# Kernel tuning notes

Measured on AMD Instinct MI355X. Metric: run time of the kernel, lower is better.

Reference implementation:

```python
import jax, jax.numpy as jnp
import numpy as np

B, BOUNDS, NRIM, K, UNITS = 4096, 512, 6, 4, 600
H_IN, DK_IN, DV_IN = 4, 64, 400
H_C, DK_C, DV_C = 4, 32, 100


def setup_inputs() -> dict:
    key = jax.random.key(0)
    ks = jax.random.split(key, 16)
    s = 0.02
    return {
        'inputs': jax.random.normal(ks[0], (B, BOUNDS + NRIM), jnp.float32),
        'hs': jax.random.normal(ks[1], (B, NRIM, UNITS), jnp.float32) * s,
        'cs': jax.random.normal(ks[2], (B, NRIM, UNITS), jnp.float32) * s,
        'Wk': jax.random.normal(ks[3], (BOUNDS, H_IN * DK_IN), jnp.float32) * s,
        'bk': jnp.zeros((H_IN * DK_IN,), jnp.float32),
        'Wv': jax.random.normal(ks[4], (BOUNDS, H_IN * DV_IN), jnp.float32) * s,
        'bv': jnp.zeros((H_IN * DV_IN,), jnp.float32),
        'Wq': jax.random.normal(ks[5], (NRIM, UNITS, H_IN * DK_IN), jnp.float32) * s,
        'lstm_k': jax.random.normal(ks[6], (NRIM, DV_IN, 4 * UNITS), jnp.float32) * s,
        'lstm_r': jax.random.normal(ks[7], (NRIM, UNITS, 4 * UNITS), jnp.float32) * s,
        'lstm_b': jnp.zeros((NRIM, 4 * UNITS), jnp.float32),
        'Wkc': jax.random.normal(ks[8], (NRIM, UNITS, H_C * DK_C), jnp.float32) * s,
        'Wvc': jax.random.normal(ks[9], (NRIM, UNITS, H_C * DV_C), jnp.float32) * s,
        'Wqc': jax.random.normal(ks[10], (NRIM, UNITS, H_C * DK_C), jnp.float32) * s,
        'Wout': jax.random.normal(ks[11], (NRIM, H_C * DV_C, UNITS), jnp.float32) * s,
    }


def _split_heads(t, n_heads, d_head):
    # [B, T, n_heads*d_head] -> [B, n_heads, T, d_head] (matches tf.split+stack)
    b, t_len = t.shape[0], t.shape[1]
    return t.reshape(b, t_len, n_heads, d_head).transpose(0, 2, 1, 3)


def reference(inputs, hs, cs, Wk, bk, Wv, bv, Wq, lstm_k, lstm_r, lstm_b, Wkc, Wvc, Wqc, Wout):
    x = inputs[:, :BOUNDS]                                   # [B, bounds]
    rim_dist = inputs[:, BOUNDS:BOUNDS + NRIM]               # [B, nRIM]

    # ---- input attention ----
    xx = jnp.stack([x, jnp.zeros_like(x)], axis=1)           # [B, 2, bounds]
    k_lay = xx @ Wk + bk                                     # [B, 2, H*dk]
    v_lay = xx @ Wv + bv                                     # [B, 2, H*dv]
    q_lay = jnp.einsum('bnu,nuo->bno', hs, Wq)               # grouped linear [B, nRIM, H*dq]
    kh = _split_heads(k_lay, H_IN, DK_IN)                    # [B, H, 2, dk]
    vh = _split_heads(v_lay, H_IN, DV_IN)                    # [B, H, 2, dv]
    qh = _split_heads(q_lay, H_IN, DK_IN)                    # [B, H, nRIM, dk]
    v2 = vh.mean(axis=1)                                     # [B, 2, dv]
    scores = jnp.einsum('bhnd,bhtd->bhnt', qh, kh) / np.sqrt(DK_IN).astype(np.float32)
    scores2 = scores.mean(axis=1)                            # [B, nRIM, 2]

    # top-k RIM selection mask from RIM_dist (use_attn=False path)
    _, idx = jax.lax.top_k(rim_dist, K)                      # [B, K]
    mask = jnp.zeros((inputs.shape[0], NRIM), inputs.dtype)
    mask = mask.at[jnp.arange(inputs.shape[0])[:, None], idx].set(1.0)[..., None]  # [B, nRIM, 1]

    probs = jax.nn.softmax(scores2, axis=-1)                 # dropout inactive (training=False)
    rnn_in = jnp.einsum('bnt,btv->bnv', probs, v2) * mask    # [B, nRIM, dv]

    # ---- grouped LSTM (keras gate order i,f,c,o) ----
    gates = (jnp.einsum('bnv,nvo->bno', rnn_in, lstm_k)
             + jnp.einsum('bnu,nuo->bno', hs, lstm_r) + lstm_b)  # [B, nRIM, 4*units]
    i, f, g, o = jnp.split(gates, 4, axis=-1)
    c_rnn = jax.nn.sigmoid(f) * cs + jax.nn.sigmoid(i) * jnp.tanh(g)
    h_rnn = jax.nn.sigmoid(o) * jnp.tanh(c_rnn)
    h_new = jax.lax.stop_gradient(h_rnn * (1.0 - mask)) + h_rnn * mask

    # ---- communication attention among RIMs ----
    kc = _split_heads(jnp.einsum('bnu,nuo->bno', h_new, Wkc), H_C, DK_C)  # [B, Hc, nRIM, dkc]
    vc = _split_heads(jnp.einsum('bnu,nuo->bno', h_new, Wvc), H_C, DV_C)
    qc = _split_heads(jnp.einsum('bnu,nuo->bno', h_new, Wqc), H_C, DK_C)
    sc = jnp.einsum('bhnd,bhmd->bhnm', qc, kc) / np.sqrt(DK_C).astype(np.float32)
    pc = jax.nn.softmax(sc, axis=-1) * mask[:, None, :, :]   # zero rows of inactive query RIMs
    ctx = jnp.einsum('bhnm,bhmv->bhnv', pc, vc)              # [B, Hc, nRIM, dvc]
    ctx = ctx.transpose(0, 2, 1, 3).reshape(inputs.shape[0], NRIM, H_C * DV_C)
    h_comm = jnp.einsum('bno,nou->bnu', ctx, Wout) + h_new   # grouped output proj + residual

    # ---- masked state update ----
    h_upd = h_comm * mask + hs * (1.0 - mask)
    c_upd = c_rnn * mask + cs * (1.0 - mask)
    out_state = h_upd.reshape(inputs.shape[0], UNITS * NRIM)
    return out_state, h_upd, c_upd
```

## Files before the change

### kernel.cpp

```cpp
#include <hip/hip_runtime.h>

namespace {
typedef unsigned short u16;
typedef __attribute__((ext_vector_type(8))) __bf16 bf16x8;
typedef __attribute__((ext_vector_type(4))) float f32x4;

constexpr long long kB  = 4096;
constexpr long long kOS = kB * 3600;

constexpr size_t oWkvT  = 0;
constexpr size_t oWqT   = oWkvT  + 768ull*512*2;
constexpr size_t oWcomT = oWqT   + 6ull*256*608*2;
constexpr size_t oWoutT = oWcomT + 6ull*768*608*2;
constexpr size_t oLstmT = oWoutT + 6ull*640*416*2;
constexpr size_t oBp    = oLstmT + 6ull*2432*1024*2;
constexpr size_t oBkv   = oBp    + 6ull*2432*4;
constexpr size_t oZero  = oBkv   + 768*4;
constexpr size_t oMask  = oZero  + 256;
constexpr size_t oArena = oMask  + 4096ull*6*4;
constexpr size_t oHs2   = oArena;
constexpr size_t oRnn   = oHs2  + (4096ull*3600+64)*2;
constexpr size_t oKV    = oRnn  + 4096ull*2400*2;
constexpr size_t oXbf   = oKV   + 4096ull*768*2;
constexpr size_t oQlay  = oXbf;
constexpr size_t oCqv   = oArena;
constexpr size_t oCtx   = oCqv  + 4096ull*4608*2;
}

__device__ __forceinline__ u16 f2b(float f) {
  union { float f; unsigned u; } x; x.f = f;
  unsigned r = (x.u + 0x7fffu + ((x.u >> 16) & 1u)) >> 16;
  return (u16)r;
}
__device__ __forceinline__ float b2f(u16 u) {
  union { unsigned u; float f; } x; x.u = ((unsigned)u) << 16;
  return x.f;
}
__device__ __forceinline__ float sigmoidf_(float x) { return 1.f / (1.f + __expf(-x)); }
__device__ __forceinline__ float tanhf_(float x) {
  const float e = __expf(2.f * x);
  return 1.f - 2.f / (e + 1.f);
}

__device__ __forceinline__ void gload16(const void* g, void* l) {
  __builtin_amdgcn_global_load_lds((const __attribute__((address_space(1))) void*)g,
                                   (__attribute__((address_space(3))) void*)l, 16, 0, 0);
}
__device__ __forceinline__ void vmcnt0_barrier() {
  asm volatile("s_waitcnt vmcnt(0)" ::: "memory");
  __builtin_amdgcn_s_barrier();
}

union FragU { uint2 u2[2]; bf16x8 v; };

template<int MODE>
__global__ __launch_bounds__(256) void gemm128(
    const u16* __restrict__ A, int lda, int strideA,
    const u16* __restrict__ A2, int lda2, int strideA2,
    const u16* __restrict__ Bt, long strideB, int Kpad,
    void* __restrict__ C, int ldc, int strideC,
    const float* __restrict__ bias, int strideBias,
    int N, int nks, int storeBf16, int nx, int swz,
    const u16* __restrict__ zerobuf,
    const float* __restrict__ cs, const float* __restrict__ mask,
    float* __restrict__ c_upd, float* __restrict__ h_upd, u16* __restrict__ hnbf,
    const float* __restrict__ hs_in, float* __restrict__ out_state)
{
  __shared__ __align__(16) u16 As0[128 * 32];
  __shared__ __align__(16) u16 Bs0[128 * 32];
  __shared__ __align__(16) u16 As1[128 * 32];
  __shared__ __align__(16) u16 Bs1[128 * 32];

  const int nwg = gridDim.x;
  const int orig = blockIdx.x;
  const int q = nwg >> 3, r = nwg & 7;
  const int xcd = orig & 7, bidx = orig >> 3;
  const int wgid = (xcd < r ? xcd * (q + 1) : r * (q + 1) + (xcd - r) * q) + bidx;
  int xt, mt, rim;
  if (swz == 0) {
    xt = wgid % nx;
    const int t2 = wgid / nx;
    mt = t2 & 31;
    rim = t2 >> 5;
  } else {
    const int g = wgid / 320;
    const int rem = wgid % 320;
    rim = g >> 1;
    mt = rem / 10;
    xt = (g & 1) * 10 + rem % 10;
    if (xt >= 19) return;
  }
  const int m0 = mt * 128, n0 = xt * 128;

  A += (size_t)rim * strideA;
  if (MODE == 2) A2 += (size_t)rim * strideA2;
  Bt += (size_t)rim * strideB;
  if (bias) bias += (size_t)rim * strideBias;

  const int t = threadIdx.x;
  const int w = t >> 6, lane = t & 63;
  const int lrow = lane & 15, lk = lane >> 4;
  const int wr = w >> 1, wc = w & 1;

  f32x4 acc[4][4] = {};

  const int rA0 = t >> 2,         cA0 = (t & 3) ^ ((rA0 >> 1) & 3);
  const int rA1 = (t + 256) >> 2, cA1 = (t & 3) ^ ((rA1 >> 1) & 3);

  auto stage = [&](int s, u16* Asd, u16* Bsd) {
    const int k0 = s * 32;
    const int gk0 = k0 + cA0 * 8, gk1 = k0 + cA1 * 8;
    const u16 *p0, *p1;
    if (MODE == 2) {
      p0 = (gk0 < 400)  ? A  + (size_t)(m0 + rA0) * lda  + gk0
         : (gk0 < 1000) ? A2 + (size_t)(m0 + rA0) * lda2 + (gk0 - 400)
                        : zerobuf;
      p1 = (gk1 < 400)  ? A  + (size_t)(m0 + rA1) * lda  + gk1
         : (gk1 < 1000) ? A2 + (size_t)(m0 + rA1) * lda2 + (gk1 - 400)
                        : zerobuf;
    } else {
      p0 = A + (size_t)(m0 + rA0) * lda + gk0;
      p1 = A + (size_t)(m0 + rA1) * lda + gk1;
    }
    gload16(p0, Asd + (size_t)t * 8);
    gload16(p1, Asd + (size_t)(t + 256) * 8);
    gload16(Bt + (size_t)(n0 + rA0) * Kpad + k0 + cA0 * 8, Bsd + (size_t)t * 8);
    gload16(Bt + (size_t)(n0 + rA1) * Kpad + k0 + cA1 * 8, Bsd + (size_t)(t + 256) * 8);
  };

  auto compute = [&](const u16* Asrc, const u16* Bsrc, int snext, u16* Asd, u16* Bsd, bool donext) {
    FragU af[4], bfr[4];
#pragma unroll
    for (int mf = 0; mf < 4; ++mf) {
      const int rr = wr * 64 + mf * 16 + lrow;
      const int sw = ((rr >> 1) & 3) << 4;
      const char* base = (const char*)Asrc + rr * 64;
      af[mf].u2[0] = *(const uint2*)(base + ((8 * lk) ^ sw));
      af[mf].u2[1] = *(const uint2*)(base + ((8 * lk + 32) ^ sw));
    }
#pragma unroll
    for (int nf = 0; nf < 4; ++nf) {
      const int rr = wc * 64 + nf * 16 + lrow;
      const int sw = ((rr >> 1) & 3) << 4;
      const char* base = (const char*)Bsrc + rr * 64;
      bfr[nf].u2[0] = *(const uint2*)(base + ((8 * lk) ^ sw));
      bfr[nf].u2[1] = *(const uint2*)(base + ((8 * lk + 32) ^ sw));
    }
    if (donext) stage(snext, Asd, Bsd);
#pragma unroll
    for (int mf = 0; mf < 4; ++mf)
#pragma unroll
      for (int nf = 0; nf < 4; ++nf)
        acc[mf][nf] = __builtin_amdgcn_mfma_f32_16x16x32_bf16(af[mf].v, bfr[nf].v, acc[mf][nf], 0, 0, 0);
    vmcnt0_barrier();
  };

  stage(0, As0, Bs0);
  vmcnt0_barrier();
  int s = 0;
  for (; s + 2 <= nks; s += 2) {
    compute(As0, Bs0, s + 1, As1, Bs1, s + 1 < nks);
    compute(As1, Bs1, s + 2, As0, Bs0, s + 2 < nks);
  }
  if (s < nks) compute(As0, Bs0, 0, As1, Bs1, false);

  if (MODE == 0) {
    float* Cf = (float*)C + (size_t)rim * strideC;
    u16*   Cu = (u16*)C + (size_t)rim * strideC;
#pragma unroll
    for (int mf = 0; mf < 4; ++mf)
#pragma unroll
      for (int r2 = 0; r2 < 4; ++r2) {
        const int m = m0 + wr * 64 + mf * 16 + 4 * lk + r2;
#pragma unroll
        for (int nf = 0; nf < 4; ++nf) {
          const int col = n0 + wc * 64 + nf * 16 + lrow;
          if (col < N) {
            float v = acc[mf][nf][r2];
            if (bias) v += bias[col];
            const size_t off = (size_t)m * ldc + col;
            if (storeBf16) Cu[off] = f2b(v); else Cf[off] = v;
          }
        }
      }
  } else if (MODE == 1) {
#pragma unroll
    for (int mf = 0; mf < 4; ++mf)
#pragma unroll
      for (int r2 = 0; r2 < 4; ++r2) {
        const int m = m0 + wr * 64 + mf * 16 + 4 * lk + r2;
        const float mk = mask[(size_t)m * 6 + rim];
#pragma unroll
        for (int nf = 0; nf < 4; ++nf) {
          const int col = n0 + wc * 64 + nf * 16 + lrow;
          if (col < 600) {
            const size_t off = (size_t)m * 3600 + rim * 600 + col;
            const float v = (mk != 0.f) ? (acc[mf][nf][r2] + h_upd[off]) : hs_in[off];
            h_upd[off] = v;
            out_state[off] = v;
          }
        }
      }
  } else {
    const int nb = n0 + wc * 64;
    const int u = ((nb >> 6) << 4) + lrow;
    if (u < 600) {
      const float bi  = bias[nb + lrow];
      const float bff = bias[nb + 16 + lrow];
      const float bg  = bias[nb + 32 + lrow];
      const float bo  = bias[nb + 48 + lrow];
#pragma unroll
      for (int mf = 0; mf < 4; ++mf)
#pragma unroll
        for (int r2 = 0; r2 < 4; ++r2) {
          const int m = m0 + wr * 64 + mf * 16 + 4 * lk + r2;
          const float iv = acc[mf][0][r2] + bi;
          const float fv = acc[mf][1][r2] + bff;
          const float gv = acc[mf][2][r2] + bg;
          const float ov = acc[mf][3][r2] + bo;
          const size_t off = (size_t)m * 3600 + rim * 600 + u;
          const float cprev = cs[off];
          const float cv = sigmoidf_(fv) * cprev + sigmoidf_(iv) * tanhf_(gv);
          const float hv = sigmoidf_(ov) * tanhf_(cv);
          const float mk = mask[(size_t)m * 6 + rim];
          c_upd[off] = (mk != 0.f) ? cv : cprev;
          h_upd[off] = hv;
          hnbf[off]  = f2b(hv);
        }
    }
  }
}

__global__ __launch_bounds__(256) void pack_wt(
    const float* __restrict__ in1, long s1,
    const float* __restrict__ in2, long s2,
    int K1, int Ktot, int ldin, int Nreal,
    u16* __restrict__ out, long so, int Kpad, int gateperm)
{
  __shared__ float tile[64][65];
  const int rim = blockIdx.z;
  const float* i1 = in1 + (size_t)rim * s1;
  const float* i2 = in2 ? in2 + (size_t)rim * s2 : nullptr;
  u16* o = out + (size_t)rim * so;
  const int n0 = blockIdx.x * 64, k0 = blockIdx.y * 64;
  const int lane = threadIdx.x & 63, qq = threadIdx.x >> 6;
  const int n = n0 + lane;
  int col;
  if (gateperm) {
    const int g = (n >> 4) & 3, u = ((n >> 6) << 4) + (n & 15);
    col = (u < 600) ? g * 600 + u : -1;
  } else {
    col = (n < Nreal) ? n : -1;
  }
#pragma unroll
  for (int i = 0; i < 16; ++i) {
    const int kk = qq + 4 * i;
    const int k = k0 + kk;
    float v = 0.f;
    if (col >= 0) {
      if (k < K1) v = i1[(size_t)k * ldin + col];
      else if (k < Ktot) v = i2[(size_t)(k - K1) * ldin + col];
    }
    tile[kk][lane] = v;
  }
  __syncthreads();
#pragma unroll
  for (int i = 0; i < 16; ++i) {
    const int nn = qq + 4 * i;
    const int k = k0 + lane;
    if (k < Kpad) o[(size_t)(n0 + nn) * Kpad + k] = f2b(tile[lane][nn]);
  }
}

__global__ void pack_kvw(const float* __restrict__ Wk, const float* __restrict__ Wv,
                         u16* __restrict__ out) {
  const int i = blockIdx.x * 256 + threadIdx.x;
  if (i >= 768 * 512) return;
  const int n = i >> 9, k = i & 511;
  float v = 0.f;
  if (n < 256) v = Wk[(size_t)k * 256 + n];
  else if (n < 656) {
    const float* p = Wv + (size_t)k * 1600 + (n - 256);
    v = 0.25f * (p[0] + p[400] + p[800] + p[1200]);
  }
  out[i] = f2b(v);
}

__global__ void pack_comw(const float* __restrict__ Wkc, const float* __restrict__ Wqc,
                          const float* __restrict__ Wvc, u16* __restrict__ out) {
  const long long i = (long long)blockIdx.x * 256 + threadIdx.x;
  if (i >= 6ll * 768 * 608) return;
  const int rim = (int)(i / (768 * 608));
  const int rem = (int)(i % (768 * 608));
  const int n = rem / 608, k = rem % 608;
  float v = 0.f;
  if (k < 600) {
    if (n < 128)      v = Wkc[(size_t)rim * 600 * 128 + (size_t)k * 128 + n];
    else if (n < 256) v = Wqc[(size_t)rim * 600 * 128 + (size_t)k * 128 + (n - 128)];
    else if (n < 656) v = Wvc[(size_t)rim * 600 * 400 + (size_t)k * 400 + (n - 256)];
  }
  out[i] = f2b(v);
}

__global__ void pack_misc(const float* __restrict__ lstm_b, const float* __restrict__ bk,
                          const float* __restrict__ bv,
                          float* __restrict__ bp, float* __restrict__ bkv, u16* __restrict__ zerobuf) {
  const int t = blockIdx.x * 256 + threadIdx.x;
  if (t < 6 * 2432) {
    const int rim = t / 2432, p = t % 2432;
    const int g = (p >> 4) & 3, u = ((p >> 6) << 4) + (p & 15);
    bp[t] = (u < 600) ? lstm_b[(size_t)rim * 2400 + g * 600 + u] : 0.f;
  }
  if (t < 768) {
    float v = 0.f;
    if (t < 256) v = bk[t];
    else if (t < 656) { const int j = t - 256; v = 0.25f * (bv[j] + bv[j + 400] + bv[j + 800] + bv[j + 1200]); }
    bkv[t] = v;
  }
  if (t < 128) zerobuf[t] = 0;
}

__global__ void pack_x(const float* __restrict__ inputs, u16* __restrict__ xbf) {
  const int idx = blockIdx.x * 256 + threadIdx.x;
  if (idx < 4096 * 512) {
    const int b = idx >> 9, c = idx & 511;
    xbf[idx] = f2b(inputs[(size_t)b * 518 + c]);
  }
}

__global__ void pack_hs2(const float* __restrict__ hs, u16* __restrict__ out) {
  const long long i8 = ((long long)blockIdx.x * 256 + threadIdx.x) * 8;
  const long long main_n = 4096ll * 3600;
  if (i8 + 8 <= main_n) {
    const float4 a = *reinterpret_cast<const float4*>(hs + i8);
    const float4 b = *reinterpret_cast<const float4*>(hs + i8 + 4);
    u16 r[8] = {f2b(a.x), f2b(a.y), f2b(a.z), f2b(a.w), f2b(b.x), f2b(b.y), f2b(b.z), f2b(b.w)};
    *reinterpret_cast<uint4*>(out + i8) = *reinterpret_cast<const uint4*>(r);
  } else if (i8 < main_n + 64) {
#pragma unroll
    for (int j = 0; j < 8; ++j) {
      const long long idx = i8 + j;
      if (idx < main_n + 64) out[idx] = f2b(idx < main_n ? hs[idx] : 0.f);
    }
  }
}

__global__ __launch_bounds__(256) void score_kernel(
    const float* __restrict__ inputs, const u16* __restrict__ qlayb,
    const u16* __restrict__ kvb, const float* __restrict__ bk,
    const float* __restrict__ bkv,
    float* __restrict__ maskout, u16* __restrict__ rnnin)
{
  const int b = blockIdx.x;
  const int t = threadIdx.x;
  __shared__ float red[4][12];
  __shared__ float sprob[12];
  __shared__ float smask[6];

  const float k0v = b2f(kvb[(size_t)b * 768 + t]);
  const float bkv_ = bk[t];
  float part[12];
#pragma unroll
  for (int n = 0; n < 6; ++n) {
    const float q = b2f(qlayb[(size_t)b * 1536 + n * 256 + t]);
    part[2 * n]     = q * k0v;
    part[2 * n + 1] = q * bkv_;
  }
#pragma unroll
  for (int off = 32; off > 0; off >>= 1)
#pragma unroll
    for (int i = 0; i < 12; ++i)
      part[i] += __shfl_down(part[i], off);
  const int wave = t >> 6, lane = t & 63;
  if (lane == 0)
#pragma unroll
    for (int i = 0; i < 12; ++i) red[wave][i] = part[i];
  __syncthreads();
  if (t < 12) red[0][t] = (red[0][t] + red[1][t] + red[2][t] + red[3][t]) * (1.0f / 32.0f);
  __syncthreads();
  if (t < 6) {
    const float s0 = red[0][2 * t], s1 = red[0][2 * t + 1];
    const float mx = fmaxf(s0, s1);
    const float e0 = __expf(s0 - mx), e1 = __expf(s1 - mx);
    const float inv = 1.f / (e0 + e1);
    sprob[2 * t] = e0 * inv;
    sprob[2 * t + 1] = e1 * inv;
    const float* rd = inputs + (size_t)b * 518 + 512;
    const float mine = rd[t];
    int rank = 0;
#pragma unroll
    for (int j = 0; j < 6; ++j) {
      const float o = rd[j];
      rank += (o > mine) || (o == mine && j < t);
    }
    const float mk = (rank < 4) ? 1.f : 0.f;
    smask[t] = mk;
    maskout[(size_t)b * 6 + t] = mk;
  }
  __syncthreads();
  for (int base = t * 4; base < 2400; base += 1024) {
    const int n = base / 400, v = base % 400;
    const float p0 = sprob[2 * n], p1 = sprob[2 * n + 1], mk = smask[n];
    ushort4 st;
    st.x = f2b((p0 * b2f(kvb[(size_t)b * 768 + 256 + v + 0]) + p1 * bkv[256 + v + 0]) * mk);
    st.y = f2b((p0 * b2f(kvb[(size_t)b * 768 + 256 + v + 1]) + p1 * bkv[256 + v + 1]) * mk);
    st.z = f2b((p0 * b2f(kvb[(size_t)b * 768 + 256 + v + 2]) + p1 * bkv[256 + v + 2]) * mk);
    st.w = f2b((p0 * b2f(kvb[(size_t)b * 768 + 256 + v + 3]) + p1 * bkv[256 + v + 3]) * mk);
    *reinterpret_cast<ushort4*>(rnnin + (size_t)b * 2400 + base) = st;
  }
}

__global__ __launch_bounds__(256) void comm_kernel(
    const u16* __restrict__ cqv, u16* __restrict__ ctx)
{
  const int b = blockIdx.x, t = threadIdx.x;
  __shared__ float skc[768], sqc[768], svc[2400];
  __shared__ float spc[4][6][6];
  for (int i = t * 4; i < 4608; i += 1024) {
    const ushort4 u4 = *reinterpret_cast<const ushort4*>(cqv + (size_t)b * 4608 + i);
    const u16 uu[4] = {u4.x, u4.y, u4.z, u4.w};
#pragma unroll
    for (int j = 0; j < 4; ++j) {
      const int ii = i + j;
      const int m = ii / 768, c = ii % 768;
      const float v = b2f(uu[j]);
      if (c < 128) skc[m * 128 + c] = v;
      else if (c < 256) sqc[m * 128 + (c - 128)] = v;
      else if (c < 656) svc[m * 400 + (c - 256)] = v;
    }
  }
  __syncthreads();
  if (t < 144) {
    const int h = t / 36, n = (t % 36) / 6, m = t % 6;
    float s = 0.f;
#pragma unroll
    for (int d = 0; d < 32; ++d) s += sqc[n * 128 + h * 32 + d] * skc[m * 128 + h * 32 + d];
    spc[h][n][m] = s * 0.17677669529663687f;
  }
  __syncthreads();
  if (t < 24) {
    const int h = t / 6, n = t % 6;
    float mx = -3.0e38f;
#pragma unroll
    for (int m = 0; m < 6; ++m) mx = fmaxf(mx, spc[h][n][m]);
    float e[6], sum = 0.f;
#pragma unroll
    for (int m = 0; m < 6; ++m) { e[m] = __expf(spc[h][n][m] - mx); sum += e[m]; }
    const float inv = 1.f / sum;
#pragma unroll
    for (int m = 0; m < 6; ++m) spc[h][n][m] = e[m] * inv;
  }
  __syncthreads();
  for (int base = t * 4; base < 2400; base += 1024) {
    const int n = base / 400, rr = base % 400, h = rr / 100, v = rr % 100;
    ushort4 st;
    float s0 = 0.f, s1 = 0.f, s2 = 0.f, s3 = 0.f;
#pragma unroll
    for (int m = 0; m < 6; ++m) {
      const float p = spc[h][n][m];
      const float* vm = &svc[m * 400 + h * 100 + v];
      s0 += p * vm[0]; s1 += p * vm[1]; s2 += p * vm[2]; s3 += p * vm[3];
    }
    st.x = f2b(s0); st.y = f2b(s1); st.z = f2b(s2); st.w = f2b(s3);
    *reinterpret_cast<ushort4*>(ctx + (size_t)b * 2400 + base) = st;
  }
}

extern "C" void kernel_launch(void* const* d_in, const int* in_sizes, int n_in,
                              void* d_out, int out_size, void* d_ws, size_t ws_size,
                              hipStream_t stream) {
  const float* inputs = (const float*)d_in[0];
  const float* hs     = (const float*)d_in[1];
  const float* cs     = (const float*)d_in[2];
  const float* Wk     = (const float*)d_in[3];
  const float* bk     = (const float*)d_in[4];
  const float* Wv     = (const float*)d_in[5];
  const float* bv     = (const float*)d_in[6];
  const float* Wq     = (const float*)d_in[7];
  const float* lstm_k = (const float*)d_in[8];
  const float* lstm_r = (const float*)d_in[9];
  const float* lstm_b = (const float*)d_in[10];
  const float* Wkc    = (const float*)d_in[11];
  const float* Wvc    = (const float*)d_in[12];
  const float* Wqc    = (const float*)d_in[13];
  const float* Wout   = (const float*)d_in[14];

  float* out = (float*)d_out;
  float* out_state = out;
  float* h_upd = out + kOS;
  float* c_upd = out + 2 * kOS;
  u16*   hnbf  = (u16*)d_out;

  char* wsb = (char*)d_ws;
  u16* WkvT  = (u16*)(wsb + oWkvT);
  u16* WqT   = (u16*)(wsb + oWqT);
  u16* WcomT = (u16*)(wsb + oWcomT);
  u16* WoutT = (u16*)(wsb + oWoutT);
  u16* LstmT = (u16*)(wsb + oLstmT);
  float* bp    = (float*)(wsb + oBp);
  float* bkv   = (float*)(wsb + oBkv);
  u16*   zerob = (u16*)(wsb + oZero);
  float* maskf = (float*)(wsb + oMask);
  u16* hs2   = (u16*)(wsb + oHs2);
  u16* rnn   = (u16*)(wsb + oRnn);
  u16* kvb   = (u16*)(wsb + oKV);
  u16* xbf   = (u16*)(wsb + oXbf);
  u16* qlayb = (u16*)(wsb + oQlay);
  u16* cqvb  = (u16*)(wsb + oCqv);
  u16* ctxb  = (u16*)(wsb + oCtx);

  dim3 B256(256);

  pack_misc<<<57, B256, 0, stream>>>(lstm_b, bk, bv, bp, bkv, zerob);
  pack_kvw<<<1536, B256, 0, stream>>>(Wk, Wv, WkvT);
  pack_comw<<<10944, B256, 0, stream>>>(Wkc, Wqc, Wvc, WcomT);
  pack_wt<<<dim3(4, 10, 6), B256, 0, stream>>>(Wq, 600ll*256, nullptr, 0, 600, 600, 256, 256, WqT, 256ll*608, 608, 0);
  pack_wt<<<dim3(10, 7, 6), B256, 0, stream>>>(Wout, 400ll*600, nullptr, 0, 400, 400, 600, 600, WoutT, 640ll*416, 416, 0);
  pack_wt<<<dim3(38, 16, 6), B256, 0, stream>>>(lstm_k, 400ll*2400, lstm_r, 600ll*2400, 400, 1000, 2400, 2400, LstmT, 2432ll*1024, 1024, 1);
  pack_x<<<8192, B256, 0, stream>>>(inputs, xbf);
  pack_hs2<<<7201, B256, 0, stream>>>(hs, hs2);

  gemm128<0><<<dim3(6*32), B256, 0, stream>>>(xbf, 512, 0, nullptr, 0, 0, WkvT, 0, 512,
      kvb, 768, 0, bkv, 0, 656, 16, 1, 6, 0, zerob,
      nullptr, nullptr, nullptr, nullptr, nullptr, nullptr, nullptr);
  gemm128<0><<<dim3(2*32*6), B256, 0, stream>>>(hs2, 3600, 600, nullptr, 0, 0, WqT, 256*608, 608,
      qlayb, 1536, 256, nullptr, 0, 256, 19, 1, 2, 0, zerob,
      nullptr, nullptr, nullptr, nullptr, nullptr, nullptr, nullptr);

  score_kernel<<<4096, B256, 0, stream>>>(inputs, qlayb, kvb, bk, bkv, maskf, rnn);

  gemm128<2><<<dim3(3840), B256, 0, stream>>>(rnn, 2400, 400, hs2, 3600, 600, LstmT, 2432l*1024, 1024,
      nullptr, 0, 0, bp, 2432, 2432, 32, 0, 10, 1, zerob,
      cs, maskf, c_upd, h_upd, hnbf, nullptr, nullptr);

  gemm128<0><<<dim3(6*32*6), B256, 0, stream>>>(hnbf, 3600, 600, nullptr, 0, 0, WcomT, 768l*608, 608,
      cqvb, 4608, 768, nullptr, 0, 656, 19, 1, 6, 0, zerob,
      nullptr, nullptr, nullptr, nullptr, nullptr, nullptr, nullptr);

  comm_kernel<<<4096, B256, 0, stream>>>(cqvb, ctxb);

  gemm128<1><<<dim3(5*32*6), B256, 0, stream>>>(ctxb, 2400, 400, nullptr, 0, 0, WoutT, 640l*416, 416,
      nullptr, 0, 0, nullptr, 0, 600, 13, 0, 5, 0, zerob,
      nullptr, maskf, nullptr, h_upd, nullptr, hs, out_state);
}
```

Measured before the change: 701.4 us.

## Use 256x128 GEMM tiles with triple-buffered LDS and a contiguous per-RIM LSTM input buffer

The GEMM kernel moves from 128x128 to 256x128 tiles, with 8x4 MFMA fragments per wave and a three-stage LDS ring whose waits use a partial vmcnt instead of a full drain every step. A new per-RIM packed A buffer (attention output followed by hs, zero-padded to 1024 columns) replaces the two-source branchy gather and the zero buffer in the LSTM GEMM. score_kernel and the new pack_gA kernel write directly into this layout. The aim is more reuse of each B tile, fewer barriers that drain all loads, and simpler address math, at the cost of more registers and LDS per block (launch bounds 256,2) and fewer workgroups for the small GEMMs.

```diff
diff --git a/kernel.cpp b/kernel.cpp
--- a/kernel.cpp
+++ b/kernel.cpp
@@ -7,6 +7,7 @@
 
 constexpr long long kB  = 4096;
 constexpr long long kOS = kB * 3600;
+constexpr size_t kGAs = 4096ull * 1024;
 
 constexpr size_t oWkvT  = 0;
 constexpr size_t oWqT   = oWkvT  + 768ull*512*2;
@@ -15,12 +16,10 @@
 constexpr size_t oLstmT = oWoutT + 6ull*640*416*2;
 constexpr size_t oBp    = oLstmT + 6ull*2432*1024*2;
 constexpr size_t oBkv   = oBp    + 6ull*2432*4;
-constexpr size_t oZero  = oBkv   + 768*4;
-constexpr size_t oMask  = oZero  + 256;
+constexpr size_t oMask  = oBkv   + 768*4;
 constexpr size_t oArena = oMask  + 4096ull*6*4;
-constexpr size_t oHs2   = oArena;
-constexpr size_t oRnn   = oHs2  + (4096ull*3600+64)*2;
-constexpr size_t oKV    = oRnn  + 4096ull*2400*2;
+constexpr size_t oGA    = oArena;
+constexpr size_t oKV    = oGA   + 6ull*kGAs*2;
 constexpr size_t oXbf   = oKV   + 4096ull*768*2;
 constexpr size_t oQlay  = oXbf;
 constexpr size_t oCqv   = oArena;
@@ -46,54 +45,34 @@
   __builtin_amdgcn_global_load_lds((const __attribute__((address_space(1))) void*)g,
                                    (__attribute__((address_space(3))) void*)l, 16, 0, 0);
 }
-__device__ __forceinline__ void vmcnt0_barrier() {
-  asm volatile("s_waitcnt vmcnt(0)" ::: "memory");
-  __builtin_amdgcn_s_barrier();
-}
 
 union FragU { uint2 u2[2]; bf16x8 v; };
 
 template<int MODE>
-__global__ __launch_bounds__(256) void gemm128(
-    const u16* __restrict__ A, int lda, int strideA,
-    const u16* __restrict__ A2, int lda2, int strideA2,
+__global__ __launch_bounds__(256, 2) void gemmP(
+    const u16* __restrict__ A, int lda, long strideA,
     const u16* __restrict__ Bt, long strideB, int Kpad,
     void* __restrict__ C, int ldc, int strideC,
     const float* __restrict__ bias, int strideBias,
-    int N, int nks, int storeBf16, int nx, int swz,
-    const u16* __restrict__ zerobuf,
+    int N, int nks, int storeBf16, int nx,
     const float* __restrict__ cs, const float* __restrict__ mask,
     float* __restrict__ c_upd, float* __restrict__ h_upd, u16* __restrict__ hnbf,
     const float* __restrict__ hs_in, float* __restrict__ out_state)
 {
-  __shared__ __align__(16) u16 As0[128 * 32];
-  __shared__ __align__(16) u16 Bs0[128 * 32];
-  __shared__ __align__(16) u16 As1[128 * 32];
-  __shared__ __align__(16) u16 Bs1[128 * 32];
+  __shared__ __align__(16) u16 lds[3 * 12288];
 
   const int nwg = gridDim.x;
   const int orig = blockIdx.x;
   const int q = nwg >> 3, r = nwg & 7;
   const int xcd = orig & 7, bidx = orig >> 3;
   const int wgid = (xcd < r ? xcd * (q + 1) : r * (q + 1) + (xcd - r) * q) + bidx;
-  int xt, mt, rim;
-  if (swz == 0) {
-    xt = wgid % nx;
-    const int t2 = wgid / nx;
-    mt = t2 & 31;
-    rim = t2 >> 5;
-  } else {
-    const int g = wgid / 320;
-    const int rem = wgid % 320;
-    rim = g >> 1;
-    mt = rem / 10;
-    xt = (g & 1) * 10 + rem % 10;
-    if (xt >= 19) return;
-  }
-  const int m0 = mt * 128, n0 = xt * 128;
+  const int mt = wgid & 15;
+  const int rest = wgid >> 4;
+  const int xt = rest % nx;
+  const int rim = rest / nx;
+  const int m0 = mt * 256, n0 = xt * 128;
 
   A += (size_t)rim * strideA;
-  if (MODE == 2) A2 += (size_t)rim * strideA2;
   Bt += (size_t)rim * strideB;
   if (bias) bias += (size_t)rim * strideBias;
 
@@ -102,39 +81,44 @@
   const int lrow = lane & 15, lk = lane >> 4;
   const int wr = w >> 1, wc = w & 1;
 
-  f32x4 acc[4][4] = {};
-
-  const int rA0 = t >> 2,         cA0 = (t & 3) ^ ((rA0 >> 1) & 3);
-  const int rA1 = (t + 256) >> 2, cA1 = (t & 3) ^ ((rA1 >> 1) & 3);
-
-  auto stage = [&](int s, u16* Asd, u16* Bsd) {
+  f32x4 acc[8][4] = {};
+
+  auto stage = [&](int s, u16* dst) {
     const int k0 = s * 32;
-    const int gk0 = k0 + cA0 * 8, gk1 = k0 + cA1 * 8;
-    const u16 *p0, *p1;
-    if (MODE == 2) {
-      p0 = (gk0 < 400)  ? A  + (size_t)(m0 + rA0) * lda  + gk0
-         : (gk0 < 1000) ? A2 + (size_t)(m0 + rA0) * lda2 + (gk0 - 400)
-                        : zerobuf;
-      p1 = (gk1 < 400)  ? A  + (size_t)(m0 + rA1) * lda  + gk1
-         : (gk1 < 1000) ? A2 + (size_t)(m0 + rA1) * lda2 + (gk1 - 400)
-                        : zerobuf;
-    } else {
-      p0 = A + (size_t)(m0 + rA0) * lda + gk0;
-      p1 = A + (size_t)(m0 + rA1) * lda + gk1;
-    }
-    gload16(p0, Asd + (size_t)t * 8);
-    gload16(p1, Asd + (size_t)(t + 256) * 8);
-    gload16(Bt + (size_t)(n0 + rA0) * Kpad + k0 + cA0 * 8, Bsd + (size_t)t * 8);
-    gload16(Bt + (size_t)(n0 + rA1) * Kpad + k0 + cA1 * 8, Bsd + (size_t)(t + 256) * 8);
+#pragma unroll
+    for (int i = 0; i < 4; ++i) {
+      const int c = t + i * 256;
+      const int rA = c >> 2, kc = (c & 3) ^ ((rA >> 1) & 3);
+      gload16(A + (size_t)(m0 + rA) * lda + k0 + kc * 8, dst + (size_t)c * 8);
+    }
+#pragma unroll
+    for (int i = 0; i < 2; ++i) {
+      const int c = t + i * 256;
+      const int rB = c >> 2, kc = (c & 3) ^ ((rB >> 1) & 3);
+      gload16(Bt + (size_t)(n0 + rB) * Kpad + k0 + kc * 8, dst + 8192 + (size_t)c * 8);
+    }
   };
 
-  auto compute = [&](const u16* Asrc, const u16* Bsrc, int snext, u16* Asd, u16* Bsd, bool donext) {
-    FragU af[4], bfr[4];
-#pragma unroll
-    for (int mf = 0; mf < 4; ++mf) {
-      const int rr = wr * 64 + mf * 16 + lrow;
+  stage(0, lds);
+  stage(1, lds + 12288);
+  int bi = 0;
+  for (int s = 0; s < nks; ++s) {
+    if (s == nks - 1) asm volatile("s_waitcnt vmcnt(0)" ::: "memory");
+    else              asm volatile("s_waitcnt vmcnt(6)" ::: "memory");
+    __builtin_amdgcn_s_barrier();
+    __builtin_amdgcn_sched_barrier(0);
+    if (s + 2 < nks) {
+      int bi2 = bi - 1; if (bi2 < 0) bi2 = 2;
+      stage(s + 2, lds + bi2 * 12288);
+    }
+    const u16* Ab = lds + bi * 12288;
+    const u16* Bb = Ab + 8192;
+    FragU af[8], bfr[4];
+#pragma unroll
+    for (int mf = 0; mf < 8; ++mf) {
+      const int rr = wr * 128 + mf * 16 + lrow;
       const int sw = ((rr >> 1) & 3) << 4;
-      const char* base = (const char*)Asrc + rr * 64;
+      const char* base = (const char*)Ab + rr * 64;
       af[mf].u2[0] = *(const uint2*)(base + ((8 * lk) ^ sw));
       af[mf].u2[1] = *(const uint2*)(base + ((8 * lk + 32) ^ sw));
     }
@@ -142,36 +126,26 @@
     for (int nf = 0; nf < 4; ++nf) {
       const int rr = wc * 64 + nf * 16 + lrow;
       const int sw = ((rr >> 1) & 3) << 4;
-      const char* base = (const char*)Bsrc + rr * 64;
+      const char* base = (const char*)Bb + rr * 64;
       bfr[nf].u2[0] = *(const uint2*)(base + ((8 * lk) ^ sw));
       bfr[nf].u2[1] = *(const uint2*)(base + ((8 * lk + 32) ^ sw));
     }
-    if (donext) stage(snext, Asd, Bsd);
-#pragma unroll
-    for (int mf = 0; mf < 4; ++mf)
+#pragma unroll
+    for (int mf = 0; mf < 8; ++mf)
 #pragma unroll
       for (int nf = 0; nf < 4; ++nf)
         acc[mf][nf] = __builtin_amdgcn_mfma_f32_16x16x32_bf16(af[mf].v, bfr[nf].v, acc[mf][nf], 0, 0, 0);
-    vmcnt0_barrier();
-  };
-
-  stage(0, As0, Bs0);
-  vmcnt0_barrier();
-  int s = 0;
-  for (; s + 2 <= nks; s += 2) {
-    compute(As0, Bs0, s + 1, As1, Bs1, s + 1 < nks);
-    compute(As1, Bs1, s + 2, As0, Bs0, s + 2 < nks);
-  }
-  if (s < nks) compute(As0, Bs0, 0, As1, Bs1, false);
+    bi = (bi == 2) ? 0 : bi + 1;
+  }
 
   if (MODE == 0) {
     float* Cf = (float*)C + (size_t)rim * strideC;
     u16*   Cu = (u16*)C + (size_t)rim * strideC;
 #pragma unroll
-    for (int mf = 0; mf < 4; ++mf)
+    for (int mf = 0; mf < 8; ++mf)
 #pragma unroll
       for (int r2 = 0; r2 < 4; ++r2) {
-        const int m = m0 + wr * 64 + mf * 16 + 4 * lk + r2;
+        const int m = m0 + wr * 128 + mf * 16 + 4 * lk + r2;
 #pragma unroll
         for (int nf = 0; nf < 4; ++nf) {
           const int col = n0 + wc * 64 + nf * 16 + lrow;
@@ -185,10 +159,10 @@
       }
   } else if (MODE == 1) {
 #pragma unroll
-    for (int mf = 0; mf < 4; ++mf)
+    for (int mf = 0; mf < 8; ++mf)
 #pragma unroll
       for (int r2 = 0; r2 < 4; ++r2) {
-        const int m = m0 + wr * 64 + mf * 16 + 4 * lk + r2;
+        const int m = m0 + wr * 128 + mf * 16 + 4 * lk + r2;
         const float mk = mask[(size_t)m * 6 + rim];
 #pragma unroll
         for (int nf = 0; nf < 4; ++nf) {
@@ -205,16 +179,16 @@
     const int nb = n0 + wc * 64;
     const int u = ((nb >> 6) << 4) + lrow;
     if (u < 600) {
-      const float bi  = bias[nb + lrow];
+      const float bi_ = bias[nb + lrow];
       const float bff = bias[nb + 16 + lrow];
       const float bg  = bias[nb + 32 + lrow];
       const float bo  = bias[nb + 48 + lrow];
 #pragma unroll
-      for (int mf = 0; mf < 4; ++mf)
+      for (int mf = 0; mf < 8; ++mf)
 #pragma unroll
         for (int r2 = 0; r2 < 4; ++r2) {
-          const int m = m0 + wr * 64 + mf * 16 + 4 * lk + r2;
-          const float iv = acc[mf][0][r2] + bi;
+          const int m = m0 + wr * 128 + mf * 16 + 4 * lk + r2;
+          const float iv = acc[mf][0][r2] + bi_;
           const float fv = acc[mf][1][r2] + bff;
           const float gv = acc[mf][2][r2] + bg;
           const float ov = acc[mf][3][r2] + bo;
@@ -304,7 +278,7 @@
 
 __global__ void pack_misc(const float* __restrict__ lstm_b, const float* __restrict__ bk,
                           const float* __restrict__ bv,
-                          float* __restrict__ bp, float* __restrict__ bkv, u16* __restrict__ zerobuf) {
+                          float* __restrict__ bp, float* __restrict__ bkv) {
   const int t = blockIdx.x * 256 + threadIdx.x;
   if (t < 6 * 2432) {
     const int rim = t / 2432, p = t % 2432;
@@ -317,7 +291,6 @@
     else if (t < 656) { const int j = t - 256; v = 0.25f * (bv[j] + bv[j + 400] + bv[j + 800] + bv[j + 1200]); }
     bkv[t] = v;
   }
-  if (t < 128) zerobuf[t] = 0;
 }
 
 __global__ void pack_x(const float* __restrict__ inputs, u16* __restrict__ xbf) {
@@ -328,20 +301,22 @@
   }
 }
 
-__global__ void pack_hs2(const float* __restrict__ hs, u16* __restrict__ out) {
-  const long long i8 = ((long long)blockIdx.x * 256 + threadIdx.x) * 8;
-  const long long main_n = 4096ll * 3600;
-  if (i8 + 8 <= main_n) {
-    const float4 a = *reinterpret_cast<const float4*>(hs + i8);
-    const float4 b = *reinterpret_cast<const float4*>(hs + i8 + 4);
-    u16 r[8] = {f2b(a.x), f2b(a.y), f2b(a.z), f2b(a.w), f2b(b.x), f2b(b.y), f2b(b.z), f2b(b.w)};
-    *reinterpret_cast<uint4*>(out + i8) = *reinterpret_cast<const uint4*>(r);
-  } else if (i8 < main_n + 64) {
-#pragma unroll
-    for (int j = 0; j < 8; ++j) {
-      const long long idx = i8 + j;
-      if (idx < main_n + 64) out[idx] = f2b(idx < main_n ? hs[idx] : 0.f);
-    }
+__global__ __launch_bounds__(256) void pack_gA(const float* __restrict__ hs, u16* __restrict__ gA) {
+  const int b = blockIdx.x, t = threadIdx.x;
+  __shared__ float row[3600];
+  for (int i = t; i < 3600; i += 256) row[i] = hs[(size_t)b * 3600 + i];
+  __syncthreads();
+  for (int c = t; c < 468; c += 256) {
+    const int rim = c / 78;
+    const int j = (c % 78) * 8;
+    u16 v[8];
+#pragma unroll
+    for (int k = 0; k < 8; ++k) {
+      const int col = j + k;
+      v[k] = (col < 600) ? f2b(row[rim * 600 + col]) : (u16)0;
+    }
+    *reinterpret_cast<uint4*>(gA + (size_t)rim * kGAs + (size_t)b * 1024 + 400 + j) =
+        *reinterpret_cast<const uint4*>(v);
   }
 }
 
@@ -349,7 +324,7 @@
     const float* __restrict__ inputs, const u16* __restrict__ qlayb,
     const u16* __restrict__ kvb, const float* __restrict__ bk,
     const float* __restrict__ bkv,
-    float* __restrict__ maskout, u16* __restrict__ rnnin)
+    float* __restrict__ maskout, u16* __restrict__ gA)
 {
   const int b = blockIdx.x;
   const int t = threadIdx.x;
@@ -398,15 +373,16 @@
     maskout[(size_t)b * 6 + t] = mk;
   }
   __syncthreads();
-  for (int base = t * 4; base < 2400; base += 1024) {
-    const int n = base / 400, v = base % 400;
+  for (int c = t; c < 300; c += 256) {
+    const int n = c / 50;
+    const int v = (c % 50) * 8;
     const float p0 = sprob[2 * n], p1 = sprob[2 * n + 1], mk = smask[n];
-    ushort4 st;
-    st.x = f2b((p0 * b2f(kvb[(size_t)b * 768 + 256 + v + 0]) + p1 * bkv[256 + v + 0]) * mk);
-    st.y = f2b((p0 * b2f(kvb[(size_t)b * 768 + 256 + v + 1]) + p1 * bkv[256 + v + 1]) * mk);
-    st.z = f2b((p0 * b2f(kvb[(size_t)b * 768 + 256 + v + 2]) + p1 * bkv[256 + v + 2]) * mk);
-    st.w = f2b((p0 * b2f(kvb[(size_t)b * 768 + 256 + v + 3]) + p1 * bkv[256 + v + 3]) * mk);
-    *reinterpret_cast<ushort4*>(rnnin + (size_t)b * 2400 + base) = st;
+    u16 st[8];
+#pragma unroll
+    for (int k = 0; k < 8; ++k)
+      st[k] = f2b((p0 * b2f(kvb[(size_t)b * 768 + 256 + v + k]) + p1 * bkv[256 + v + k]) * mk);
+    *reinterpret_cast<uint4*>(gA + (size_t)n * kGAs + (size_t)b * 1024 + v) =
+        *reinterpret_cast<const uint4*>(st);
   }
 }
 
@@ -499,10 +475,8 @@
   u16* LstmT = (u16*)(wsb + oLstmT);
   float* bp    = (float*)(wsb + oBp);
   float* bkv   = (float*)(wsb + oBkv);
-  u16*   zerob = (u16*)(wsb + oZero);
   float* maskf = (float*)(wsb + oMask);
-  u16* hs2   = (u16*)(wsb + oHs2);
-  u16* rnn   = (u16*)(wsb + oRnn);
+  u16* gA    = (u16*)(wsb + oGA);
   u16* kvb   = (u16*)(wsb + oKV);
   u16* xbf   = (u16*)(wsb + oXbf);
   u16* qlayb = (u16*)(wsb + oQlay);
@@ -511,35 +485,35 @@
 
   dim3 B256(256);
 
-  pack_misc<<<57, B256, 0, stream>>>(lstm_b, bk, bv, bp, bkv, zerob);
+  pack_misc<<<57, B256, 0, stream>>>(lstm_b, bk, bv, bp, bkv);
   pack_kvw<<<1536, B256, 0, stream>>>(Wk, Wv, WkvT);
   pack_comw<<<10944, B256, 0, stream>>>(Wkc, Wqc, Wvc, WcomT);
   pack_wt<<<dim3(4, 10, 6), B256, 0, stream>>>(Wq, 600ll*256, nullptr, 0, 600, 600, 256, 256, WqT, 256ll*608, 608, 0);
   pack_wt<<<dim3(10, 7, 6), B256, 0, stream>>>(Wout, 400ll*600, nullptr, 0, 400, 400, 600, 600, WoutT, 640ll*416, 416, 0);
   pack_wt<<<dim3(38, 16, 6), B256, 0, stream>>>(lstm_k, 400ll*2400, lstm_r, 600ll*2400, 400, 1000, 2400, 2400, LstmT, 2432ll*1024, 1024, 1);
   pack_x<<<8192, B256, 0, stream>>>(inputs, xbf);
-  pack_hs2<<<7201, B256, 0, stream>>>(hs, hs2);
-
-  gemm128<0><<<dim3(6*32), B256, 0, stream>>>(xbf, 512, 0, nullptr, 0, 0, WkvT, 0, 512,
-      kvb, 768, 0, bkv, 0, 656, 16, 1, 6, 0, zerob,
+  pack_gA<<<4096, B256, 0, stream>>>(hs, gA);
+
+  gemmP<0><<<dim3(96), B256, 0, stream>>>(xbf, 512, 0, WkvT, 0, 512,
+      kvb, 768, 0, bkv, 0, 656, 16, 1, 6,
       nullptr, nullptr, nullptr, nullptr, nullptr, nullptr, nullptr);
-  gemm128<0><<<dim3(2*32*6), B256, 0, stream>>>(hs2, 3600, 600, nullptr, 0, 0, WqT, 256*608, 608,
-      qlayb, 1536, 256, nullptr, 0, 256, 19, 1, 2, 0, zerob,
+  gemmP<0><<<dim3(192), B256, 0, stream>>>(gA + 400, 1024, (long)kGAs, WqT, 256l*608, 608,
+      qlayb, 1536, 256, nullptr, 0, 256, 19, 1, 2,
       nullptr, nullptr, nullptr, nullptr, nullptr, nullptr, nullptr);
 
-  score_kernel<<<4096, B256, 0, stream>>>(inputs, qlayb, kvb, bk, bkv, maskf, rnn);
-
-  gemm128<2><<<dim3(3840), B256, 0, stream>>>(rnn, 2400, 400, hs2, 3600, 600, LstmT, 2432l*1024, 1024,
-      nullptr, 0, 0, bp, 2432, 2432, 32, 0, 10, 1, zerob,
+  score_kernel<<<4096, B256, 0, stream>>>(inputs, qlayb, kvb, bk, bkv, maskf, gA);
+
+  gemmP<2><<<dim3(1824), B256, 0, stream>>>(gA, 1024, (long)kGAs, LstmT, 2432l*1024, 1024,
+      nullptr, 0, 0, bp, 2432, 2432, 32, 0, 19,
       cs, maskf, c_upd, h_upd, hnbf, nullptr, nullptr);
 
-  gemm128<0><<<dim3(6*32*6), B256, 0, stream>>>(hnbf, 3600, 600, nullptr, 0, 0, WcomT, 768l*608, 608,
-      cqvb, 4608, 768, nullptr, 0, 656, 19, 1, 6, 0, zerob,
+  gemmP<0><<<dim3(576), B256, 0, stream>>>(hnbf, 3600, 600, WcomT, 768l*608, 608,
+      cqvb, 4608, 768, nullptr, 0, 656, 19, 1, 6,
       nullptr, nullptr, nullptr, nullptr, nullptr, nullptr, nullptr);
 
   comm_kernel<<<4096, B256, 0, stream>>>(cqvb, ctxb);
 
-  gemm128<1><<<dim3(5*32*6), B256, 0, stream>>>(ctxb, 2400, 400, nullptr, 0, 0, WoutT, 640l*416, 416,
-      nullptr, 0, 0, nullptr, 0, 600, 13, 0, 5, 0, zerob,
+  gemmP<1><<<dim3(480), B256, 0, stream>>>(ctxb, 2400, 400, WoutT, 640l*416, 416,
+      nullptr, 0, 0, nullptr, 0, 600, 13, 0, 5,
       nullptr, maskf, nullptr, h_upd, nullptr, hs, out_state);
 }
```

Measured after the change: 706.8 us. About the same (+0.8%).
